# Performance work log

Hardware: AMD Instinct MI355X
Metric: run time of the kernel (lower is better)

## Reference

```python
import jax, jax.numpy as jnp
import numpy as np

B, IMG, P, C = 32, 224, 16, 3
D, H, HD, F, L, NC = 768, 12, 64, 3072, 12, 1000
NP = (IMG // P) ** 2  # 196 patches


def setup_inputs() -> dict:
    key = jax.random.key(0)
    ks = iter(jax.random.split(key, 40))
    rn = lambda shape, s=0.02: jax.random.normal(next(ks), shape, jnp.float32) * s
    inp = {"images": jax.random.normal(next(ks), (B, IMG, IMG, C), jnp.float32)}
    inp["patch_W"] = rn((P * P * C, D)); inp["patch_b"] = jnp.zeros((D,), jnp.float32)
    inp["pos_emb"] = rn((NP, D)); inp["cls"] = rn((1, 1, D))
    inp["ln1_g"] = jnp.ones((L, D), jnp.float32); inp["ln1_b"] = jnp.zeros((L, D), jnp.float32)
    inp["Wq"] = rn((L, H, D, HD)); inp["bq"] = jnp.zeros((L, H, HD), jnp.float32)
    inp["Wk"] = rn((L, H, D, HD)); inp["bk"] = jnp.zeros((L, H, HD), jnp.float32)
    inp["Wv"] = rn((L, H, D, HD)); inp["bv"] = jnp.zeros((L, H, HD), jnp.float32)
    inp["Wo"] = rn((L, H * HD, D)); inp["bo"] = jnp.zeros((L, D), jnp.float32)
    inp["ln2_g"] = jnp.ones((L, D), jnp.float32); inp["ln2_b"] = jnp.zeros((L, D), jnp.float32)
    inp["W1"] = rn((L, D, F)); inp["b1"] = jnp.zeros((L, F), jnp.float32)
    inp["W2"] = rn((L, F, D)); inp["b2"] = jnp.zeros((L, D), jnp.float32)
    inp["head_g"] = jnp.ones((D,), jnp.float32); inp["head_bn"] = jnp.zeros((D,), jnp.float32)
    inp["head_W"] = rn((D, NC)); inp["head_bias"] = jnp.zeros((NC,), jnp.float32)
    return inp


def _ln(x, g, b, eps=1e-5):
    m = jnp.mean(x, axis=-1, keepdims=True)
    v = jnp.var(x, axis=-1, keepdims=True)
    return (x - m) * jax.lax.rsqrt(v + eps) * g + b


def reference(images, patch_W, patch_b, pos_emb, cls, ln1_g, ln1_b, Wq, bq, Wk, bk, Wv, bv, Wo, bo, ln2_g, ln2_b, W1, b1, W2, b2, head_g, head_bn, head_W, head_bias):
    Bn = images.shape[0]
    n = IMG // P
    # patch extraction: [B, n, P, n, P, C] -> [B, n*n, P*P*C] (row-major within patch, like tf.image.extract_patches)
    patches = images.reshape(Bn, n, P, n, P, C).transpose(0, 1, 3, 2, 4, 5).reshape(Bn, NP, P * P * C)
    x = patches @ patch_W + patch_b + pos_emb[None]  # pos emb added before cls concat (as in source)
    x = jnp.concatenate([jnp.broadcast_to(cls, (Bn, 1, D)), x], axis=1)  # [B, NP+1, D]
    scale = 1.0 / jnp.sqrt(jnp.float32(HD))
    for l in range(L):
        xn = _ln(x, ln1_g[l], ln1_b[l])
        q = jnp.einsum('bsd,hde->bhse', xn, Wq[l]) + bq[l][None, :, None, :]
        k = jnp.einsum('bsd,hde->bhse', xn, Wk[l]) + bk[l][None, :, None, :]
        v = jnp.einsum('bsd,hde->bhse', xn, Wv[l]) + bv[l][None, :, None, :]
        att = jax.nn.softmax(jnp.einsum('bhqe,bhke->bhqk', q, k) * scale, axis=-1)
        o = jnp.einsum('bhqk,bhke->bhqe', att, v)
        o = o.transpose(0, 2, 1, 3).reshape(Bn, -1, H * HD)  # concat heads
        x = x + o @ Wo[l] + bo[l]
        h = _ln(x, ln2_g[l], ln2_b[l])
        h = jax.nn.gelu(h @ W1[l] + b1[l], approximate=False)  # tf.nn.gelu default is exact
        x = x + h @ W2[l] + b2[l]
    logits = _ln(x[:, 0, :], head_g, head_bn) @ head_W + head_bias
    return logits
```

## Files before the change

kernel.cpp:

```cpp
#include <hip/hip_runtime.h>
#include <hip/hip_bf16.h>
#include <math.h>

#define S_LEN   197
#define NPATCH  196
#define BATCHSZ 32
#define DMODEL  768
#define NHEAD   12
#define HDIM    64
#define FFDIM   3072
#define NLAYER  12
#define NCLS    1000
#define NTOK    (BATCHSZ * S_LEN)

#define FLAG_BIAS    1
#define FLAG_RESID   2
#define FLAG_GELU    4
#define FLAG_OUTBF16 8

typedef __attribute__((ext_vector_type(8))) short short8;
typedef __attribute__((ext_vector_type(4))) float f32x4;
typedef __hip_bfloat16 bf16;

#define GLOBAL_AS __attribute__((address_space(1)))
#define LDS_AS    __attribute__((address_space(3)))

static __device__ __forceinline__ short bf16bits(float x) {
    bf16 b = __float2bfloat16(x);
    return *reinterpret_cast<short*>(&b);
}

__global__ __launch_bounds__(256) void extract_patches_k(
    const float* __restrict__ images, bf16* __restrict__ patches)
{
    int r = blockIdx.x;
    int b = r / NPATCH, p = r - b * NPATCH;
    int i = p / 14, j = p - i * 14;
    int tid = threadIdx.x;
#pragma unroll
    for (int t = 0; t < 3; ++t) {
        int k = tid + t * 256;
        int pi = k / 48;
        int rem = k - pi * 48;
        int pj = rem / 3;
        int c  = rem - pj * 3;
        long long src = (((long long)(b * 224 + i * 16 + pi)) * 224 + (j * 16 + pj)) * 3 + c;
        patches[(long long)r * 768 + k] = __float2bfloat16(images[src]);
    }
}

__global__ __launch_bounds__(256) void embed_k(
    const float* __restrict__ ptmp, const float* __restrict__ pos,
    const float* __restrict__ cls, float* __restrict__ x)
{
    long long idx = (long long)blockIdx.x * 256 + threadIdx.x;
    int d = idx % DMODEL;
    long long r = idx / DMODEL;
    int b = r / S_LEN, s = r - (long long)b * S_LEN;
    float v;
    if (s == 0) v = cls[d];
    else v = ptmp[((long long)b * NPATCH + s - 1) * DMODEL + d] + pos[(long long)(s - 1) * DMODEL + d];
    x[idx] = v;
}

__global__ __launch_bounds__(256) void transpose_conv_k(
    const float* __restrict__ src, bf16* __restrict__ dst, int R, int C)
{
    __shared__ float t[32][33];
    int tx = threadIdx.x & 31, ty = threadIdx.x >> 5;
    int c0 = blockIdx.x * 32, r0 = blockIdx.y * 32;
#pragma unroll
    for (int i = 0; i < 4; ++i) {
        int r = r0 + ty + i * 8;
        if (r < R && c0 + tx < C) t[ty + i * 8][tx] = src[(long long)r * C + c0 + tx];
    }
    __syncthreads();
#pragma unroll
    for (int i = 0; i < 4; ++i) {
        int c = c0 + ty + i * 8;
        if (c < C && r0 + tx < R) dst[(long long)c * R + r0 + tx] = __float2bfloat16(t[tx][ty + i * 8]);
    }
}

__global__ __launch_bounds__(256) void conv_layer_k(
    const float* __restrict__ Wq, const float* __restrict__ Wk, const float* __restrict__ Wv,
    const float* __restrict__ Wo, const float* __restrict__ W1, const float* __restrict__ W2,
    const float* __restrict__ bq, const float* __restrict__ bk, const float* __restrict__ bv,
    bf16* __restrict__ wqkv_t, bf16* __restrict__ wo_t,
    bf16* __restrict__ w1_t, bf16* __restrict__ w2_t, float* __restrict__ bqkv)
{
    int t = blockIdx.x;
    int tid = threadIdx.x;
    if (t == 6912) {
        for (int i = tid; i < 2304; i += 256) {
            int m = i / 768, r = i - m * 768;
            bqkv[i] = (m == 0 ? bq : m == 1 ? bk : bv)[r];
        }
        return;
    }
    const float* src; bf16* dst;
    int C; long long dld;
    int r0, c0;
    if (t < 1728) {
        int slab = t / 48, rem = t - slab * 48;
        int mat = slab / 12, h = slab - mat * 12;
        src = (mat == 0 ? Wq : mat == 1 ? Wk : Wv) + (long long)h * 768 * 64;
        dst = wqkv_t + ((long long)mat * 768 + h * 64) * 768;
        C = 64; dld = 768;
        r0 = (rem >> 1) * 32; c0 = (rem & 1) * 32;
    } else if (t < 2304) {
        int rem = t - 1728;
        src = Wo; dst = wo_t; C = 768; dld = 768;
        r0 = (rem / 24) * 32; c0 = (rem % 24) * 32;
    } else if (t < 4608) {
        int rem = t - 2304;
        src = W1; dst = w1_t; C = 3072; dld = 768;
        r0 = (rem / 96) * 32; c0 = (rem % 96) * 32;
    } else {
        int rem = t - 4608;
        src = W2; dst = w2_t; C = 768; dld = 3072;
        r0 = (rem / 24) * 32; c0 = (rem % 24) * 32;
    }
    __shared__ float tile[32][33];
    int tx = tid & 31, ty = tid >> 5;
#pragma unroll
    for (int i = 0; i < 4; ++i)
        tile[ty + i * 8][tx] = src[(long long)(r0 + ty + i * 8) * C + c0 + tx];
    __syncthreads();
#pragma unroll
    for (int i = 0; i < 4; ++i)
        dst[(long long)(c0 + ty + i * 8) * dld + r0 + tx] = __float2bfloat16(tile[tx][ty + i * 8]);
}

__global__ __launch_bounds__(256) void vt_k(
    const bf16* __restrict__ qkv, bf16* __restrict__ Vt)
{
    int z = blockIdx.z;
    int b = z / NHEAD, h = z - b * NHEAD;
    int s0 = blockIdx.x * 32, e0 = blockIdx.y * 32;
    __shared__ bf16 t[32][33];
    int tx = threadIdx.x & 31, ty = threadIdx.x >> 5;
#pragma unroll
    for (int i = 0; i < 4; ++i) {
        int s = s0 + ty + i * 8;
        bf16 v = __float2bfloat16(0.f);
        if (s < S_LEN) v = qkv[((long long)(b * S_LEN + s)) * 2304 + 1536 + h * 64 + e0 + tx];
        t[ty + i * 8][tx] = v;
    }
    __syncthreads();
#pragma unroll
    for (int i = 0; i < 4; ++i) {
        int e = e0 + ty + i * 8;
        Vt[((long long)z * 64 + e) * 224 + s0 + tx] = t[tx][ty + i * 8];
    }
}

__global__ __launch_bounds__(256) void ln_k(
    const float* __restrict__ xin, long long instride,
    const float* __restrict__ g, const float* __restrict__ b,
    float* __restrict__ xout, long long outstride)
{
    int row = blockIdx.x;
    const float* xr = xin + (long long)row * instride;
    float* orow = xout + (long long)row * outstride;
    int tid = threadIdx.x;
    float v0 = xr[tid], v1 = xr[tid + 256], v2 = xr[tid + 512];
    __shared__ float s[256];
    s[tid] = v0 + v1 + v2;
    __syncthreads();
    for (int st = 128; st > 0; st >>= 1) { if (tid < st) s[tid] += s[tid + st]; __syncthreads(); }
    float mean = s[0] * (1.0f / DMODEL);
    __syncthreads();
    float d0 = v0 - mean, d1 = v1 - mean, d2 = v2 - mean;
    s[tid] = d0 * d0 + d1 * d1 + d2 * d2;
    __syncthreads();
    for (int st = 128; st > 0; st >>= 1) { if (tid < st) s[tid] += s[tid + st]; __syncthreads(); }
    float rs = rsqrtf(s[0] * (1.0f / DMODEL) + 1e-5f);
    orow[tid]       = d0 * rs * g[tid]       + b[tid];
    orow[tid + 256] = d1 * rs * g[tid + 256] + b[tid + 256];
    orow[tid + 512] = d2 * rs * g[tid + 512] + b[tid + 512];
}

__global__ __launch_bounds__(256) void ln_bf_k(
    const float* __restrict__ xin, long long instride,
    const float* __restrict__ g, const float* __restrict__ b,
    bf16* __restrict__ xout, long long outstride)
{
    int row = blockIdx.x;
    const float* xr = xin + (long long)row * instride;
    bf16* orow = xout + (long long)row * outstride;
    int tid = threadIdx.x;
    float v0 = xr[tid], v1 = xr[tid + 256], v2 = xr[tid + 512];
    __shared__ float s[256];
    s[tid] = v0 + v1 + v2;
    __syncthreads();
    for (int st = 128; st > 0; st >>= 1) { if (tid < st) s[tid] += s[tid + st]; __syncthreads(); }
    float mean = s[0] * (1.0f / DMODEL);
    __syncthreads();
    float d0 = v0 - mean, d1 = v1 - mean, d2 = v2 - mean;
    s[tid] = d0 * d0 + d1 * d1 + d2 * d2;
    __syncthreads();
    for (int st = 128; st > 0; st >>= 1) { if (tid < st) s[tid] += s[tid + st]; __syncthreads(); }
    float rs = rsqrtf(s[0] * (1.0f / DMODEL) + 1e-5f);
    orow[tid]       = __float2bfloat16(d0 * rs * g[tid]       + b[tid]);
    orow[tid + 256] = __float2bfloat16(d1 * rs * g[tid + 256] + b[tid + 256]);
    orow[tid + 512] = __float2bfloat16(d2 * rs * g[tid + 512] + b[tid + 512]);
}

__global__ __launch_bounds__(256) void attn_k(
    const bf16* __restrict__ qkvb, const bf16* __restrict__ Vtb,
    bf16* __restrict__ Ob)
{
    __shared__ short KP[14336];
    __shared__ short Vs[14336];

    int tid = threadIdx.x;
    int lane = tid & 63, wid = tid >> 6;
    int rl = lane & 15, quad = lane >> 4;
    int qb = blockIdx.x;
    int z = blockIdx.y;
    int b = z / NHEAD, h = z - b * NHEAD;
    const short* qg = (const short*)qkvb;
    const short* vg = (const short*)Vtb;

#pragma unroll
    for (int c = 0; c < 7; ++c) {
        int f = wid * 7 + c;
        if (f < 26) {
            int jn = f >> 1, s = f & 1;
            int krow = jn * 16 + rl; if (krow > 196) krow = 196;
            const short* src = qg + ((long long)(b * S_LEN + krow) * 2304 + 768 + h * 64 + s * 32 + quad * 8);
            __builtin_amdgcn_global_load_lds((GLOBAL_AS const void*)src,
                                             (LDS_AS void*)&KP[f * 512], 16, 0, 0);
        }
        {
            int et = f / 7, s2 = f - et * 7;
            int e = et * 16 + rl;
            const short* src = vg + ((long long)(z * 64 + e) * 224 + s2 * 32 + quad * 8);
            __builtin_amdgcn_global_load_lds((GLOBAL_AS const void*)src,
                                             (LDS_AS void*)&Vs[f * 512], 16, 0, 0);
        }
    }
    int qrow = qb * 64 + wid * 16 + rl;
    int qrc = qrow > 196 ? 196 : qrow;
    long long qbase = (long long)(b * S_LEN + qrc) * 2304 + h * 64 + quad * 8;
    short8 q0 = *(const short8*)(qg + qbase);
    short8 q1 = *(const short8*)(qg + qbase + 32);
    __syncthreads();

    f32x4 accS[13];
#pragma unroll
    for (int jn = 0; jn < 13; ++jn) accS[jn] = (f32x4){0.f, 0.f, 0.f, 0.f};
#pragma unroll
    for (int jn = 0; jn < 13; ++jn) {
        short8 b0 = *(const short8*)&KP[(jn * 2 + 0) * 512 + lane * 8];
        short8 b1 = *(const short8*)&KP[(jn * 2 + 1) * 512 + lane * 8];
        accS[jn] = __builtin_amdgcn_mfma_f32_16x16x32_bf16(q0, b0, accS[jn], 0, 0, 0);
        accS[jn] = __builtin_amdgcn_mfma_f32_16x16x32_bf16(q1, b1, accS[jn], 0, 0, 0);
    }
    __syncthreads();

    float mx[4] = {-1e30f, -1e30f, -1e30f, -1e30f};
    float sm[4] = {0.f, 0.f, 0.f, 0.f};
#pragma unroll
    for (int r = 0; r < 4; ++r) {
#pragma unroll
        for (int jn = 0; jn < 13; ++jn) {
            int col = jn * 16 + rl;
            if (col < S_LEN) mx[r] = fmaxf(mx[r], accS[jn][r] * 0.125f);
        }
#pragma unroll
        for (int d = 1; d < 16; d <<= 1) mx[r] = fmaxf(mx[r], __shfl_xor(mx[r], d, 64));
    }
    float pv[13][4];
#pragma unroll
    for (int jn = 0; jn < 13; ++jn) {
        int col = jn * 16 + rl;
#pragma unroll
        for (int r = 0; r < 4; ++r) {
            float p = (col < S_LEN) ? __expf(accS[jn][r] * 0.125f - mx[r]) : 0.f;
            pv[jn][r] = p;
            sm[r] += p;
        }
    }
#pragma unroll
    for (int r = 0; r < 4; ++r) {
#pragma unroll
        for (int d = 1; d < 16; d <<= 1) sm[r] += __shfl_xor(sm[r], d, 64);
        sm[r] = 1.0f / sm[r];
    }

    int pbase = wid * 7 * 512;
#pragma unroll
    for (int jn = 0; jn < 13; ++jn) {
        int col = jn * 16 + rl;
        int s2 = col >> 5, kk = col & 31;
        int lidx = (kk >> 3) * 16, j = kk & 7;
#pragma unroll
        for (int r = 0; r < 4; ++r) {
            int m = quad * 4 + r;
            KP[pbase + s2 * 512 + (m + lidx) * 8 + j] = bf16bits(pv[jn][r] * sm[r]);
        }
    }
    {
        int col = 208 + rl;
        int kk = col & 31;
        int lidx = (kk >> 3) * 16, j = kk & 7;
#pragma unroll
        for (int r = 0; r < 4; ++r) {
            int m = quad * 4 + r;
            KP[pbase + 6 * 512 + (m + lidx) * 8 + j] = 0;
        }
    }

    short8 pa[7];
#pragma unroll
    for (int s2 = 0; s2 < 7; ++s2) pa[s2] = *(const short8*)&KP[pbase + s2 * 512 + lane * 8];
    f32x4 accO[4];
#pragma unroll
    for (int et = 0; et < 4; ++et) accO[et] = (f32x4){0.f, 0.f, 0.f, 0.f};
#pragma unroll
    for (int et = 0; et < 4; ++et)
#pragma unroll
        for (int s2 = 0; s2 < 7; ++s2) {
            short8 bb = *(const short8*)&Vs[(et * 7 + s2) * 512 + lane * 8];
            accO[et] = __builtin_amdgcn_mfma_f32_16x16x32_bf16(pa[s2], bb, accO[et], 0, 0, 0);
        }

#pragma unroll
    for (int et = 0; et < 4; ++et) {
        int e = et * 16 + rl;
#pragma unroll
        for (int r = 0; r < 4; ++r) {
            int q = qb * 64 + wid * 16 + quad * 4 + r;
            if (q < S_LEN)
                Ob[((long long)(b * S_LEN + q)) * DMODEL + h * 64 + e] = __float2bfloat16(accO[et][r]);
        }
    }
}

__global__ __launch_bounds__(256) void head_k(
    const float* __restrict__ xcls, const float* __restrict__ W,
    const float* __restrict__ bias, float* __restrict__ out)
{
    int nt = blockIdx.x, b = blockIdx.y;
    int tid = threadIdx.x;
    int nl = tid & 63, kq = tid >> 6;
    int n = nt * 64 + nl;
    __shared__ float xs[DMODEL];
    for (int i = tid; i < DMODEL; i += 256) xs[i] = xcls[(long long)b * DMODEL + i];
    __syncthreads();
    float sum = 0.f;
    if (n < NCLS) {
        const float* Wp = W + (long long)kq * 192 * NCLS + n;
#pragma unroll 8
        for (int k = 0; k < 192; ++k)
            sum = fmaf(xs[kq * 192 + k], Wp[(long long)k * NCLS], sum);
    }
    __shared__ float red[256];
    red[tid] = sum;
    __syncthreads();
    if (kq == 0 && n < NCLS)
        out[(long long)b * NCLS + n] = red[nl] + red[nl + 64] + red[nl + 128] + red[nl + 192] + bias[n];
}

__global__ __launch_bounds__(256) void resid2_k(
    const float* __restrict__ t0, const float* __restrict__ t1,
    const float* __restrict__ b2, float* __restrict__ x)
{
    long long i = (long long)blockIdx.x * 256 + threadIdx.x;
    int col4 = i % (DMODEL / 4);
    const f32x4* t0v = (const f32x4*)t0;
    const f32x4* t1v = (const f32x4*)t1;
    const f32x4* b2v = (const f32x4*)b2;
    f32x4* xv = (f32x4*)x;
    f32x4 v = xv[i];
    f32x4 a = t0v[i], b = t1v[i], c = b2v[col4];
    v.x += a.x + b.x + c.x;
    v.y += a.y + b.y + c.y;
    v.z += a.z + b.z + c.z;
    v.w += a.w + b.w + c.w;
    xv[i] = v;
}

__global__ __launch_bounds__(256) void mfma_gemm_k(
    const bf16* __restrict__ A, const bf16* __restrict__ Bt,
    const float* __restrict__ bias, const float* __restrict__ resid,
    float* __restrict__ Cf, bf16* __restrict__ Cb,
    int M, int N, int K, int lda, int ldb, int ldc, int ldr,
    long long zA, long long zB, long long zC, int flags)
{
    __shared__ short As[4096];
    __shared__ short Bs[4096];

    int tid = threadIdx.x;
    int lane = tid & 63, wid = tid >> 6;
    int wm = wid & 1, wn = wid >> 1;
    long long block_m = (long long)blockIdx.y * 128;
    long long block_n = (long long)blockIdx.x * 128;
    int zz = blockIdx.z;

    const short* Ag = (const short*)A + zz * zA;
    const short* Bg = (const short*)Bt + zz * zB;
    if (Cf) Cf += zz * zC;
    if (Cb) Cb += zz * zC;

    int rl   = lane & 15;
    int koff = (lane >> 4) * 8;

    f32x4 acc[4][4] = {};

    for (int k0 = 0; k0 < K; k0 += 32) {
#pragma unroll
        for (int c = 0; c < 4; ++c) {
            int bi = wid * 4 + c;
            int rloc = (bi & 7) * 16 + rl;
            const short* src;
            short* dst;
            if (bi < 8) {
                long long grow = block_m + rloc;
                if (grow >= M) grow = M - 1;
                src = Ag + grow * lda + k0 + koff;
                dst = &As[bi * 512];
            } else {
                long long grow = block_n + rloc;
                src = Bg + grow * ldb + k0 + koff;
                dst = &Bs[(bi - 8) * 512];
            }
            __builtin_amdgcn_global_load_lds((GLOBAL_AS const void*)src,
                                             (LDS_AS void*)dst, 16, 0, 0);
        }
        __syncthreads();

        short8 a[4], b[4];
        const short8* ap = (const short8*)As;
        const short8* bp = (const short8*)Bs;
#pragma unroll
        for (int i = 0; i < 4; ++i) a[i] = ap[(wm * 4 + i) * 64 + lane];
#pragma unroll
        for (int j = 0; j < 4; ++j) b[j] = bp[(wn * 4 + j) * 64 + lane];
#pragma unroll
        for (int i = 0; i < 4; ++i)
#pragma unroll
            for (int j = 0; j < 4; ++j)
                acc[i][j] = __builtin_amdgcn_mfma_f32_16x16x32_bf16(a[i], b[j], acc[i][j], 0, 0, 0);
        __syncthreads();
    }

    int cl = lane & 15;
    int rq = (lane >> 4) * 4;
#pragma unroll
    for (int j = 0; j < 4; ++j) {
        long long col = block_n + wn * 64 + j * 16 + cl;
        float bv = (flags & FLAG_BIAS) ? bias[col] : 0.f;
#pragma unroll
        for (int i = 0; i < 4; ++i) {
#pragma unroll
            for (int r = 0; r < 4; ++r) {
                long long row = block_m + wm * 64 + i * 16 + rq + r;
                if (row >= M) continue;
                float v = acc[i][j][r] + bv;
                if (flags & FLAG_GELU) v = 0.5f * v * (1.0f + erff(v * 0.70710678118f));
                if (flags & FLAG_RESID) v += resid[row * (long long)ldr + col];
                if (flags & FLAG_OUTBF16) Cb[row * (long long)ldc + col] = __float2bfloat16(v);
                else Cf[row * (long long)ldc + col] = v;
            }
        }
    }
}

static inline void launch_mfma(hipStream_t stream,
    const bf16* A, const bf16* Bt, const float* bias, const float* resid,
    float* Cf, bf16* Cb, int M, int N, int K, int ldc, int ldr, int flags)
{
    dim3 grid(N / 128, (M + 127) / 128, 1);
    mfma_gemm_k<<<grid, dim3(256), 0, stream>>>(A, Bt, bias, resid, Cf, Cb,
        M, N, K, K, K, ldc, ldr, 0, 0, 0, flags);
}

extern "C" void kernel_launch(void* const* d_in, const int* in_sizes, int n_in,
                              void* d_out, int out_size, void* d_ws, size_t ws_size,
                              hipStream_t stream)
{
    const float* images   = (const float*)d_in[0];
    const float* patch_W  = (const float*)d_in[1];
    const float* patch_b  = (const float*)d_in[2];
    const float* pos_emb  = (const float*)d_in[3];
    const float* cls      = (const float*)d_in[4];
    const float* ln1_g    = (const float*)d_in[5];
    const float* ln1_b    = (const float*)d_in[6];
    const float* Wq       = (const float*)d_in[7];
    const float* bq       = (const float*)d_in[8];
    const float* Wk       = (const float*)d_in[9];
    const float* bk       = (const float*)d_in[10];
    const float* Wv       = (const float*)d_in[11];
    const float* bv       = (const float*)d_in[12];
    const float* Wo       = (const float*)d_in[13];
    const float* bo       = (const float*)d_in[14];
    const float* ln2_g    = (const float*)d_in[15];
    const float* ln2_b    = (const float*)d_in[16];
    const float* W1       = (const float*)d_in[17];
    const float* b1       = (const float*)d_in[18];
    const float* W2       = (const float*)d_in[19];
    const float* b2       = (const float*)d_in[20];
    const float* head_g   = (const float*)d_in[21];
    const float* head_bn  = (const float*)d_in[22];
    const float* head_W   = (const float*)d_in[23];
    const float* head_bias= (const float*)d_in[24];
    float* out = (float*)d_out;

    char* p = (char*)d_ws;
    auto alloc = [&](long long nbytes) { char* r = p; p += (nbytes + 255) & ~255LL; return r; };
    const long long SZ = (long long)NTOK * DMODEL;

    float* x      = (float*)alloc(SZ * 4);
    bf16*  xn     = (bf16*) alloc(SZ * 2);
    bf16*  qkvb   = (bf16*) alloc((long long)NTOK * 2304 * 2);
    float* ptmp   = (float*)qkvb;
    bf16*  Vt     = (bf16*) alloc((long long)384 * 64 * 224 * 2);
    bf16*  h1     = (bf16*) alloc((long long)NTOK * FFDIM * 2);
    float* w2tmp  = (float*)alloc(2 * SZ * 4);
    bf16*  Ob     = (bf16*) alloc(SZ * 2);
    bf16*  patches= Ob;
    bf16*  wqkv_t = (bf16*) alloc((long long)2304 * 768 * 2);
    bf16*  wo_t   = (bf16*) alloc((long long)768 * 768 * 2);
    bf16*  w1_t   = (bf16*) alloc((long long)3072 * 768 * 2);
    bf16*  w2_t   = (bf16*) alloc((long long)768 * 3072 * 2);
    bf16*  pw_t   = (bf16*) alloc((long long)768 * 768 * 2);
    float* bqkv   = (float*)alloc(2304 * 4);
    float* xcls   = (float*)alloc((long long)BATCHSZ * DMODEL * 4);

    extract_patches_k<<<dim3(BATCHSZ * NPATCH), dim3(256), 0, stream>>>(images, patches);
    transpose_conv_k<<<dim3(24, 24), dim3(256), 0, stream>>>(patch_W, pw_t, 768, 768);
    launch_mfma(stream, patches, pw_t, patch_b, nullptr, ptmp, nullptr,
                BATCHSZ * NPATCH, DMODEL, 768, DMODEL, 0, FLAG_BIAS);
    embed_k<<<dim3((int)(SZ / 256)), dim3(256), 0, stream>>>(ptmp, pos_emb, cls, x);

    const long long WQKV_L = (long long)NHEAD * DMODEL * HDIM;
    for (int l = 0; l < NLAYER; ++l) {
        conv_layer_k<<<dim3(6913), dim3(256), 0, stream>>>(
            Wq + (long long)l * WQKV_L, Wk + (long long)l * WQKV_L, Wv + (long long)l * WQKV_L,
            Wo + (long long)l * DMODEL * DMODEL,
            W1 + (long long)l * DMODEL * FFDIM,
            W2 + (long long)l * FFDIM * DMODEL,
            bq + (long long)l * 768, bk + (long long)l * 768, bv + (long long)l * 768,
            wqkv_t, wo_t, w1_t, w2_t, bqkv);

        ln_bf_k<<<dim3(NTOK), dim3(256), 0, stream>>>(
            x, DMODEL, ln1_g + l * DMODEL, ln1_b + l * DMODEL, xn, DMODEL);

        launch_mfma(stream, xn, wqkv_t, bqkv, nullptr, nullptr, qkvb,
                    NTOK, 2304, DMODEL, 2304, 0, FLAG_BIAS | FLAG_OUTBF16);

        vt_k<<<dim3(7, 2, 384), dim3(256), 0, stream>>>(qkvb, Vt);

        attn_k<<<dim3(4, 384), dim3(256), 0, stream>>>(qkvb, Vt, Ob);

        launch_mfma(stream, Ob, wo_t, bo + (long long)l * DMODEL, x, x, nullptr,
                    NTOK, DMODEL, DMODEL, DMODEL, DMODEL, FLAG_BIAS | FLAG_RESID);

        ln_bf_k<<<dim3(NTOK), dim3(256), 0, stream>>>(
            x, DMODEL, ln2_g + l * DMODEL, ln2_b + l * DMODEL, xn, DMODEL);

        launch_mfma(stream, xn, w1_t, b1 + (long long)l * FFDIM, nullptr, nullptr, h1,
                    NTOK, FFDIM, DMODEL, FFDIM, 0, FLAG_BIAS | FLAG_GELU | FLAG_OUTBF16);

        {
            dim3 grid(DMODEL / 128, (NTOK + 127) / 128, 2);
            mfma_gemm_k<<<grid, dim3(256), 0, stream>>>(
                h1, w2_t, nullptr, nullptr, w2tmp, nullptr,
                NTOK, DMODEL, 1536, FFDIM, FFDIM, DMODEL, 0,
                1536, 1536, SZ, 0);
            resid2_k<<<dim3((int)(SZ / 4 / 256)), dim3(256), 0, stream>>>(
                w2tmp, w2tmp + SZ, b2 + (long long)l * DMODEL, x);
        }
    }

    ln_k<<<dim3(BATCHSZ), dim3(256), 0, stream>>>(
        x, (long long)S_LEN * DMODEL, head_g, head_bn, xcls, DMODEL);
    head_k<<<dim3(16, BATCHSZ), dim3(256), 0, stream>>>(xcls, head_W, head_bias, out);
}
```

Baseline: 5.006 ms.

## Triple-buffer GEMM LDS loads, remap workgroups per XCD, use tanh-form GELU

Measured after the change: 4.432 ms. 11.5% less time.

```diff
diff --git a/kernel.cpp b/kernel.cpp
--- a/kernel.cpp
+++ b/kernel.cpp
@@ -390,51 +390,84 @@
     int M, int N, int K, int lda, int ldb, int ldc, int ldr,
     long long zA, long long zB, long long zC, int flags)
 {
-    __shared__ short As[4096];
-    __shared__ short Bs[4096];
+    __shared__ short As[3 * 4096];
+    __shared__ short Bs[3 * 4096];
 
     int tid = threadIdx.x;
     int lane = tid & 63, wid = tid >> 6;
     int wm = wid & 1, wn = wid >> 1;
-    long long block_m = (long long)blockIdx.y * 128;
-    long long block_n = (long long)blockIdx.x * 128;
-    int zz = blockIdx.z;
-
-    const short* Ag = (const short*)A + zz * zA;
-    const short* Bg = (const short*)Bt + zz * zB;
-    if (Cf) Cf += zz * zC;
-    if (Cb) Cb += zz * zC;
+
+    int gx = gridDim.x, gy = gridDim.y;
+    int nwg = gx * gy * gridDim.z;
+    int lin = blockIdx.x + gx * (blockIdx.y + gy * blockIdx.z);
+    int q8 = nwg >> 3, r8 = nwg & 7;
+    int xcd = lin & 7, idx = lin >> 3;
+    int wg = (xcd < r8) ? (xcd * (q8 + 1) + idx)
+                        : (r8 * (q8 + 1) + (xcd - r8) * q8 + idx);
+    int by = wg % gy;
+    int t2 = wg / gy;
+    int bx = t2 % gx;
+    int bz = t2 / gx;
+
+    long long block_m = (long long)by * 128;
+    long long block_n = (long long)bx * 128;
+
+    const short* Ag = (const short*)A + (long long)bz * zA;
+    const short* Bg = (const short*)Bt + (long long)bz * zB;
+    if (Cf) Cf += (long long)bz * zC;
+    if (Cb) Cb += (long long)bz * zC;
 
     int rl   = lane & 15;
-    int koff = (lane >> 4) * 8;
+    int quad = lane >> 4;
+
+    const short* srcp[4];
+    short* dstb[4];
+#pragma unroll
+    for (int c = 0; c < 4; ++c) {
+        int bi = wid * 4 + c;
+        int f = bi & 7;
+        if (bi < 8) {
+            long long grow = block_m + f * 16 + rl;
+            if (grow >= M) grow = M - 1;
+            srcp[c] = Ag + grow * lda + quad * 8;
+            dstb[c] = &As[f * 512];
+        } else {
+            long long grow = block_n + f * 16 + rl;
+            srcp[c] = Bg + grow * ldb + quad * 8;
+            dstb[c] = &Bs[f * 512];
+        }
+    }
+
+#define STAGE(BUF) do {                                                        \
+    _Pragma("unroll")                                                          \
+    for (int c = 0; c < 4; ++c) {                                              \
+        __builtin_amdgcn_global_load_lds((GLOBAL_AS const void*)srcp[c],       \
+            (LDS_AS void*)(dstb[c] + (BUF) * 4096), 16, 0, 0);                 \
+        srcp[c] += 32;                                                         \
+    } } while (0)
 
     f32x4 acc[4][4] = {};
 
-    for (int k0 = 0; k0 < K; k0 += 32) {
-#pragma unroll
-        for (int c = 0; c < 4; ++c) {
-            int bi = wid * 4 + c;
-            int rloc = (bi & 7) * 16 + rl;
-            const short* src;
-            short* dst;
-            if (bi < 8) {
-                long long grow = block_m + rloc;
-                if (grow >= M) grow = M - 1;
-                src = Ag + grow * lda + k0 + koff;
-                dst = &As[bi * 512];
-            } else {
-                long long grow = block_n + rloc;
-                src = Bg + grow * ldb + k0 + koff;
-                dst = &Bs[(bi - 8) * 512];
-            }
-            __builtin_amdgcn_global_load_lds((GLOBAL_AS const void*)src,
-                                             (LDS_AS void*)dst, 16, 0, 0);
-        }
-        __syncthreads();
-
+    int nt = K >> 5;
+    STAGE(0);
+    STAGE(1);
+    int sbuf = 2, cbuf = 0;
+
+    for (int t = 0; t < nt; ++t) {
+        if (t + 2 < nt) {
+            STAGE(sbuf);
+            sbuf = (sbuf == 2) ? 0 : sbuf + 1;
+            asm volatile("s_waitcnt vmcnt(8)" ::: "memory");
+        } else if (t + 1 < nt) {
+            asm volatile("s_waitcnt vmcnt(4)" ::: "memory");
+        } else {
+            asm volatile("s_waitcnt vmcnt(0)" ::: "memory");
+        }
+        __builtin_amdgcn_s_barrier();
+
+        const short8* ap = (const short8*)(As + cbuf * 4096);
+        const short8* bp = (const short8*)(Bs + cbuf * 4096);
         short8 a[4], b[4];
-        const short8* ap = (const short8*)As;
-        const short8* bp = (const short8*)Bs;
 #pragma unroll
         for (int i = 0; i < 4; ++i) a[i] = ap[(wm * 4 + i) * 64 + lane];
 #pragma unroll
@@ -444,23 +477,33 @@
 #pragma unroll
             for (int j = 0; j < 4; ++j)
                 acc[i][j] = __builtin_amdgcn_mfma_f32_16x16x32_bf16(a[i], b[j], acc[i][j], 0, 0, 0);
-        __syncthreads();
-    }
+
+        __builtin_amdgcn_s_barrier();
+        cbuf = (cbuf == 2) ? 0 : cbuf + 1;
+    }
+#undef STAGE
 
     int cl = lane & 15;
     int rq = (lane >> 4) * 4;
-#pragma unroll
-    for (int j = 0; j < 4; ++j) {
-        long long col = block_n + wn * 64 + j * 16 + cl;
-        float bv = (flags & FLAG_BIAS) ? bias[col] : 0.f;
-#pragma unroll
-        for (int i = 0; i < 4; ++i) {
-#pragma unroll
-            for (int r = 0; r < 4; ++r) {
-                long long row = block_m + wm * 64 + i * 16 + rq + r;
-                if (row >= M) continue;
-                float v = acc[i][j][r] + bv;
-                if (flags & FLAG_GELU) v = 0.5f * v * (1.0f + erff(v * 0.70710678118f));
+    float bv[4];
+#pragma unroll
+    for (int j = 0; j < 4; ++j)
+        bv[j] = (flags & FLAG_BIAS) ? bias[block_n + wn * 64 + j * 16 + cl] : 0.f;
+
+#pragma unroll
+    for (int i = 0; i < 4; ++i) {
+#pragma unroll
+        for (int r = 0; r < 4; ++r) {
+            long long row = block_m + wm * 64 + i * 16 + rq + r;
+            if (row >= M) continue;
+#pragma unroll
+            for (int j = 0; j < 4; ++j) {
+                long long col = block_n + wn * 64 + j * 16 + cl;
+                float v = acc[i][j][r] + bv[j];
+                if (flags & FLAG_GELU) {
+                    float z = 1.5957691216f * v * (1.0f + 0.044715f * v * v);
+                    v = v / (1.0f + __expf(-z));
+                }
                 if (flags & FLAG_RESID) v += resid[row * (long long)ldr + col];
                 if (flags & FLAG_OUTBF16) Cb[row * (long long)ldc + col] = __float2bfloat16(v);
                 else Cf[row * (long long)ldc + col] = v;
```
